# Performance work log

Hardware: AMD Instinct MI355X
Metric: run time of the kernel (lower is better)

## Reference

```python
import jax, jax.numpy as jnp
import numpy as np

T, B, K, N, M = 1024, 32, 8, 64, 64
DELTA = 3  # number of passes: DELTA-1 states-only + 1 final with output


def setup_inputs():
    key = jax.random.key(0)
    ks = jax.random.split(key, 7)
    x = jax.random.normal(ks[0], (T, B, K), jnp.float32)
    # stable, a.s.-distinct complex eigenvalues: |lam| in [0.5, 0.99)
    mag = jax.random.uniform(ks[1], (K, N), jnp.float32, 0.5, 0.99)
    phase = jax.random.uniform(ks[2], (K, N), jnp.float32, -np.pi, np.pi)
    lam_re = mag * jnp.cos(phase)
    lam_im = mag * jnp.sin(phase)
    C_re = jax.random.normal(ks[3], (K, N, M), jnp.float32) / np.sqrt(N)
    C_im = jax.random.normal(ks[4], (K, N, M), jnp.float32) / np.sqrt(N)
    D = jax.random.normal(ks[5], (K, M), jnp.float32)
    Do = jax.random.normal(ks[6], (K, M), jnp.float32)
    return {"x": x, "lam_re": lam_re, "lam_im": lam_im,
            "C_re": C_re, "C_im": C_im, "D": D, "Do": Do}


def _compute_Bp(lam):
    # Bʹ[k,j] = exp(-sum_i log(1 - lam_i/lam_j)), diagonal ratio zeroed
    k, n = lam.shape
    ratios = lam[:, :, None] / lam[:, None, :]           # (k, n, n)
    eye = jnp.eye(n, dtype=bool)[None]
    ratios = jnp.where(eye, jnp.zeros((), ratios.dtype), ratios)
    lnBp = -jnp.sum(jnp.log(1.0 - ratios), axis=1)       # (k, n)
    return jnp.exp(lnBp)


def _linear_recurrence(a, bx):
    # s_t = a_t * s_{t-1} + bx_t, computed as a parallel associative scan
    def comb(l, r):
        al, bl = l
        ar, br = r
        return (al * ar, bl * ar + br)
    _, s = jax.lax.associative_scan(comb, (a, bx), axis=0)
    return s


def _states(xc, lam, Bp, alpha):
    # one pass of the complex diagonal SSM; returns states (T, B, K, N)
    Bpx = (xc[..., None] * Bp).reshape(T, B, K * N)       # Bʹ·x
    if alpha is None:
        al = jnp.broadcast_to(lam.reshape(1, 1, K * N), (T, B, K * N))
    else:
        al = (alpha * lam[None, None]).reshape(T, B, K * N)  # α·λ
    # standard=True: shift inputs by one step (prepend zeros, drop last)
    z = jnp.zeros((1, B, K * N), al.dtype)
    al = jnp.concatenate([z, al[:-1]], axis=0)
    Bpx = jnp.concatenate([z, Bpx[:-1]], axis=0)
    return _linear_recurrence(al, Bpx).reshape(T, B, K, N)


def _forward(x, lam_re, lam_im, C_re, C_im, D, Do):
    lam = (lam_re + 1j * lam_im).astype(jnp.complex64)    # (K, N)
    Cp = (C_re + 1j * C_im).astype(jnp.complex64)         # (K, N, M)
    xc = x.astype(jnp.complex64)                          # (T, B, K)
    Bp = _compute_Bp(lam)                                 # (K, N)

    alpha = None
    for _ in range(DELTA - 1):
        s = _states(xc, lam, Bp, alpha)                   # (T, B, K, N)
        ls = lam[None, None] * s                          # λ·sʹ
        alpha = 1.0 / jnp.sqrt(1.0 + ls * jnp.conj(ls))   # recipsq

    s = _states(xc, lam, Bp, alpha)                       # final pass
    Cs = jnp.einsum("tbkn,knm->tbkm", s, Cp)              # Cʹ·sʹ
    Dx = xc[..., None] * D.astype(jnp.complex64)          # D·x
    y = Cs + Dx + Do.astype(jnp.complex64)                # (T, B, K, M)
    return jnp.mean(y, axis=2)                            # average over k


def reference(x, lam_re, lam_im, C_re, C_im, D, Do):
    return _forward(x, lam_re, lam_im, C_re, C_im, D, Do)
```

## Files before the change

### kernel.cpp

```cpp
#include <hip/hip_runtime.h>

#define TT 1024
#define BB 32
#define KKD 8
#define NN 64
#define MM 64
#define BKC (BB*KKD)
#define KN  (KKD*NN)

typedef __attribute__((ext_vector_type(8))) _Float16 f16x8;
typedef __attribute__((ext_vector_type(2))) __fp16 fp16x2;
typedef __attribute__((ext_vector_type(4))) float f32x4;

#define SC_DOWN (1.0f/4096.0f)
#define SC_UP   512.0f


static __device__ __forceinline__ float bcast(float v, int lane) {
    return __builtin_bit_cast(float,
        __builtin_amdgcn_readlane(__builtin_bit_cast(int, v), lane));
}
static __device__ __forceinline__ float f16lo(unsigned int pk) {
    return (float)__builtin_bit_cast(_Float16, (unsigned short)(pk & 0xffffu));
}
static __device__ __forceinline__ float f16hi(unsigned int pk) {
    return (float)__builtin_bit_cast(_Float16, (unsigned short)(pk >> 16));
}

__global__ __launch_bounds__(64) void bp_kernel(const float* __restrict__ lam_re,
                                                const float* __restrict__ lam_im,
                                                float* __restrict__ bp) {
    int k = blockIdx.x;
    int j = threadIdx.x;
    double ljre = (double)lam_re[k*NN+j], ljim = (double)lam_im[k*NN+j];
    double dj = ljre*ljre + ljim*ljim;
    double pre = 1.0, pim = 0.0;
    for (int i = 0; i < NN; ++i) {
        if (i == j) continue;
        double lire = (double)lam_re[k*NN+i], liim = (double)lam_im[k*NN+i];
        double rre = (lire*ljre + liim*ljim)/dj;
        double rim = (liim*ljre - lire*ljim)/dj;
        double zre = 1.0 - rre, zim = -rim;
        double zd = zre*zre + zim*zim;
        double npre = (pre*zre + pim*zim)/zd;
        double npim = (pim*zre - pre*zim)/zd;
        pre = npre; pim = npim;
    }
    bp[(k*NN+j)*2+0] = (float)pre;
    bp[(k*NN+j)*2+1] = (float)pim;
}

__global__ __launch_bounds__(256) void wprep_kernel(const float* __restrict__ C_re,
                                                    const float* __restrict__ C_im,
                                                    unsigned short* __restrict__ Wt) {
    int idx = blockIdx.x*256 + threadIdx.x;
    int m  = idx >> 10;
    int j  = idx & 1023;
    int kn = j >> 1;
    float v = (j & 1) ? -C_im[kn*MM + m] : C_re[kn*MM + m];
    Wt[idx] = __builtin_bit_cast(unsigned short, (_Float16)(v * SC_UP));
}

__global__ __launch_bounds__(512, 8) void scan_par5_kernel(const float* __restrict__ x,
                                                           const float* __restrict__ lam_re,
                                                           const float* __restrict__ lam_im,
                                                           const float* __restrict__ bp,
                                                           unsigned int* __restrict__ abuf,
                                                           int TL) {
    __shared__ float e[32][16][2];
    __shared__ float pa[32][16];
    __shared__ unsigned int apk[32][16][17];

    int blk = blockIdx.x;
    int bk = blk >> 2;
    int q2 = blk & 3;
    int b = bk >> 3;
    int k = bk & 7;
    int tid = threadIdx.x;
    int seg = tid >> 4;
    int nl  = tid & 15;
    int n   = q2*16 + nl;
    int kn  = k*NN + n;

    float lre = lam_re[kn], lim = lam_im[kn];
    float bpre = bp[2*kn+0], bpim = bp[2*kn+1];
    float l2 = lre*lre + lim*lim;

    float p32re = lre, p32im = lim;
    #pragma unroll
    for (int i = 0; i < 5; ++i) {
        float tr = p32re*p32re - p32im*p32im;
        float ti = 2.f*p32re*p32im;
        p32re = tr; p32im = ti;
    }

    float xs0 = x[(size_t)(seg*32 + nl)*BKC + b*KKD + k];
    float xs1 = x[(size_t)(seg*32 + 16 + nl)*BKC + b*KKD + k];

    float s1re = 0.f, s1im = 0.f;
    #pragma unroll
    for (int i = 0; i < 32; ++i) {
        float xv = (i < 16) ? __shfl(xs0, i, 16) : __shfl(xs1, i - 16, 16);
        float ure = xv*bpre, uim = xv*bpim;
        float tre = __builtin_fmaf(lre, s1re, __builtin_fmaf(-lim, s1im, ure));
        float tim = __builtin_fmaf(lre, s1im, __builtin_fmaf( lim, s1re, uim));
        s1re = tre; s1im = tim;
    }
    e[seg][nl][0] = s1re; e[seg][nl][1] = s1im;
    __syncthreads();
    float c1re = 0.f, c1im = 0.f;
    for (int i = 0; i < seg; ++i) {
        float tre = __builtin_fmaf(p32re, c1re, __builtin_fmaf(-p32im, c1im, e[i][nl][0]));
        float tim = __builtin_fmaf(p32re, c1im, __builtin_fmaf( p32im, c1re, e[i][nl][1]));
        c1re = tre; c1im = tim;
    }
    __syncthreads();

    s1re = c1re; s1im = c1im;
    float s2re = 0.f, s2im = 0.f, pav = 1.f;
    float a1prev = 0.f;
    #pragma unroll
    for (int i = 0; i < 32; ++i) {
        float xv = (i < 16) ? __shfl(xs0, i, 16) : __shfl(xs1, i - 16, 16);
        float ure = xv*bpre, uim = xv*bpim;
        float mm1 = __builtin_fmaf(l2, __builtin_fmaf(s1re, s1re, s1im*s1im), 1.f);
        float a1 = rsqrtf(mm1);
        float t1re = __builtin_fmaf(lre, s1re, __builtin_fmaf(-lim, s1im, ure));
        float t1im = __builtin_fmaf(lre, s1im, __builtin_fmaf( lim, s1re, uim));
        s1re = t1re; s1im = t1im;
        float cr = a1*lre, ci = a1*lim;
        float t2re = __builtin_fmaf(cr, s2re, __builtin_fmaf(-ci, s2im, ure));
        float t2im = __builtin_fmaf(cr, s2im, __builtin_fmaf( ci, s2re, uim));
        s2re = t2re; s2im = t2im;
        pav *= a1;
        if (i & 1)
            apk[seg][i>>1][nl] = __builtin_bit_cast(unsigned int,
                                   __builtin_amdgcn_cvt_pkrtz(a1prev, a1));
        else
            a1prev = a1;
    }
    e[seg][nl][0] = s2re; e[seg][nl][1] = s2im; pa[seg][nl] = pav;
    __syncthreads();
    float c2re = 0.f, c2im = 0.f;
    for (int i = 0; i < seg; ++i) {
        float pai = pa[i][nl];
        float qre = pai*p32re, qim = pai*p32im;
        float tre = __builtin_fmaf(qre, c2re, __builtin_fmaf(-qim, c2im, e[i][nl][0]));
        float tim = __builtin_fmaf(qre, c2im, __builtin_fmaf( qim, c2re, e[i][nl][1]));
        c2re = tre; c2im = tim;
    }
    __syncthreads();

    s2re = c2re; s2im = c2im;
    float s3re = 0.f, s3im = 0.f, pb = 1.f;
    float a2prev = 0.f;
    unsigned int pk = 0;
    #pragma unroll
    for (int i = 0; i < 32; ++i) {
        if (!(i & 1)) pk = apk[seg][i>>1][nl];
        float a1 = (i & 1) ? f16hi(pk) : f16lo(pk);
        float xv = (i < 16) ? __shfl(xs0, i, 16) : __shfl(xs1, i - 16, 16);
        float ure = xv*bpre, uim = xv*bpim;
        float mm2 = __builtin_fmaf(l2, __builtin_fmaf(s2re, s2re, s2im*s2im), 1.f);
        float a2 = rsqrtf(mm2);
        float cr = a1*lre, ci = a1*lim;
        float t2re = __builtin_fmaf(cr, s2re, __builtin_fmaf(-ci, s2im, ure));
        float t2im = __builtin_fmaf(cr, s2im, __builtin_fmaf( ci, s2re, uim));
        s2re = t2re; s2im = t2im;
        float dr = a2*lre, di = a2*lim;
        float t3re = __builtin_fmaf(dr, s3re, __builtin_fmaf(-di, s3im, ure));
        float t3im = __builtin_fmaf(dr, s3im, __builtin_fmaf( di, s3re, uim));
        s3re = t3re; s3im = t3im;
        pb *= a2;
        if (i & 1)
            apk[seg][i>>1][nl] = __builtin_bit_cast(unsigned int,
                                   __builtin_amdgcn_cvt_pkrtz(a2prev, a2));
        else
            a2prev = a2;
    }
    e[seg][nl][0] = s3re; e[seg][nl][1] = s3im; pa[seg][nl] = pb;
    __syncthreads();
    float c3re = 0.f, c3im = 0.f;
    for (int i = 0; i < seg; ++i) {
        float pbi = pa[i][nl];
        float qre = pbi*p32re, qim = pbi*p32im;
        float tre = __builtin_fmaf(qre, c3re, __builtin_fmaf(-qim, c3im, e[i][nl][0]));
        float tim = __builtin_fmaf(qre, c3im, __builtin_fmaf( qim, c3re, e[i][nl][1]));
        c3re = tre; c3im = tim;
    }

    s3re = c3re; s3im = c3im;
    unsigned int* ap = abuf + (size_t)(bk*4 + q2)*((size_t)TL*16)
                     + (seg >> 2)*2048 + (seg & 3)*16 + nl;
    #pragma unroll
    for (int i = 0; i < 32; ++i) {
        fp16x2 hv = __builtin_amdgcn_cvt_pkrtz(s3re*SC_DOWN, s3im*SC_DOWN);
        ap[(size_t)i * 64] = __builtin_bit_cast(unsigned int, hv);
        if (!(i & 1)) pk = apk[seg][i>>1][nl];
        float a2 = (i & 1) ? f16hi(pk) : f16lo(pk);
        float xv = (i < 16) ? __shfl(xs0, i, 16) : __shfl(xs1, i - 16, 16);
        float ure = xv*bpre, uim = xv*bpim;
        float dr = a2*lre, di = a2*lim;
        float t3re = __builtin_fmaf(dr, s3re, __builtin_fmaf(-di, s3im, ure));
        float t3im = __builtin_fmaf(dr, s3im, __builtin_fmaf( di, s3re, uim));
        s3re = t3re; s3im = t3im;
    }
}

__global__ __launch_bounds__(64) void scan_seq_kernel(const float* __restrict__ x,
                                                      const float* __restrict__ lam_re,
                                                      const float* __restrict__ lam_im,
                                                      const float* __restrict__ bp,
                                                      float* __restrict__ state,
                                                      unsigned int* __restrict__ abuf,
                                                      int chunk_start, int chunk_len,
                                                      int TL) {
    int bk = blockIdx.x;
    int b = bk >> 3;
    int k = bk & 7;
    int n = threadIdx.x;
    int kn = k*NN + n;
    float lre = lam_re[kn], lim = lam_im[kn];
    float bpre = bp[2*kn+0], bpim = bp[2*kn+1];
    float l2 = lre*lre + lim*lim;
    int chain = bk*NN + n;

    float s1re,s1im,s2re,s2im,s3re,s3im;
    if (chunk_start == 0) {
        s1re=s1im=s2re=s2im=s3re=s3im=0.f;
    } else {
        const float* st = state + (size_t)chain*6;
        s1re=st[0];s1im=st[1];s2re=st[2];s2im=st[3];s3re=st[4];s3im=st[5];
    }

    const float* xp = x + (size_t)chunk_start*BKC + b*KKD + k;
    int q2_ = n >> 4, nl_ = n & 15;
    unsigned int* ab = abuf + (size_t)(bk*4 + q2_)*((size_t)TL*16) + nl_;

    float xs = xp[(size_t)n * BKC];
    for (int t0 = 0; t0 < chunk_len; t0 += 64) {
        float xs_nxt = 0.f;
        if (t0 + 64 < chunk_len) xs_nxt = xp[(size_t)(t0 + 64 + n) * BKC];
        #pragma unroll
        for (int w = 0; w < 4; ++w) {
            float mm_[16], cre[16], cim[16];
            #pragma unroll
            for (int j = 0; j < 16; ++j) {
                float xv = bcast(xs, w*16 + j);
                mm_[j] = __builtin_fmaf(l2, s1re*s1re + s1im*s1im, 1.0f);
                float ure = xv*bpre, uim = xv*bpim;
                float tre = __builtin_fmaf(lre, s1re, __builtin_fmaf(-lim, s1im, ure));
                float tim = __builtin_fmaf(lre, s1im, __builtin_fmaf( lim, s1re, uim));
                s1re=tre; s1im=tim;
            }
            #pragma unroll
            for (int j = 0; j < 16; ++j) {
                float a = rsqrtf(mm_[j]); cre[j] = a*lre; cim[j] = a*lim;
            }
            #pragma unroll
            for (int j = 0; j < 16; ++j) {
                float xv = bcast(xs, w*16 + j);
                mm_[j] = __builtin_fmaf(l2, s2re*s2re + s2im*s2im, 1.0f);
                float ure = xv*bpre, uim = xv*bpim;
                float tre = __builtin_fmaf(cre[j], s2re, __builtin_fmaf(-cim[j], s2im, ure));
                float tim = __builtin_fmaf(cre[j], s2im, __builtin_fmaf( cim[j], s2re, uim));
                s2re=tre; s2im=tim;
            }
            #pragma unroll
            for (int j = 0; j < 16; ++j) {
                float a = rsqrtf(mm_[j]); cre[j] = a*lre; cim[j] = a*lim;
            }
            #pragma unroll
            for (int j = 0; j < 16; ++j) {
                int t = t0 + w*16 + j;
                fp16x2 hv = __builtin_amdgcn_cvt_pkrtz(s3re*SC_DOWN, s3im*SC_DOWN);
                ab[((size_t)(t >> 7))*2048 + (t & 31)*64 + ((t >> 5) & 3)*16]
                    = __builtin_bit_cast(unsigned int, hv);
                float xv = bcast(xs, w*16 + j);
                float ure = xv*bpre, uim = xv*bpim;
                float tre = __builtin_fmaf(cre[j], s3re, __builtin_fmaf(-cim[j], s3im, ure));
                float tim = __builtin_fmaf(cre[j], s3im, __builtin_fmaf( cim[j], s3re, uim));
                s3re=tre; s3im=tim;
            }
        }
        xs = xs_nxt;
    }
    float* st = state + (size_t)chain*6;
    st[0]=s1re;st[1]=s1im;st[2]=s2re;st[3]=s2im;st[4]=s3re;st[5]=s3im;
}

__global__ __launch_bounds__(256) void proj_kernel(const unsigned int* __restrict__ A,
                                                   const unsigned short* __restrict__ Wt,
                                                   const float* __restrict__ x,
                                                   const float* __restrict__ D,
                                                   const float* __restrict__ Do,
                                                   float* __restrict__ out,
                                                   int rowOff, int TL) {
    __shared__ uint4 At[2][1024];
    __shared__ uint4 Wb[2][1024];
    int tid = threadIdx.x;
    int w = tid >> 6, l = tid & 63;
    int lg = l >> 4, lr = l & 15;
    int wr = w >> 1, wc = w & 1;
    int bI = blockIdx.x;
    int t0 = ((bI >> 5) << 6) + (bI & 31);
    size_t TLQ = (size_t)TL * 16;

    f32x4 acc[2][2];
    #pragma unroll
    for (int g = 0; g < 2; ++g)
        #pragma unroll
        for (int t = 0; t < 2; ++t) acc[g][t] = (f32x4){0.f,0.f,0.f,0.f};

    uint4 ra[4], rw[4];
    int srow[4], su[4];
    #pragma unroll
    for (int i = 0; i < 4; ++i) {
        int unit = w*256 + i*64 + l;
        srow[i] = unit >> 4;
        su[i]   = unit & 15;
    }

    #pragma unroll
    for (int i = 0; i < 4; ++i) {
        int row = srow[i], u = su[i];
        int b = row & 31, t2 = t0 + ((row >> 5) << 5);
        size_t idx = (size_t)((b*8 + 0)*4 + (u >> 2))*TLQ
                   + (size_t)(t2 >> 7)*2048 + (t2 & 31)*64 + ((t2 >> 5) & 3)*16 + (u & 3)*4;
        ra[i] = *(const uint4*)(A + idx);
        rw[i] = *(const uint4*)((const char*)Wt + (row*2048 + 0*256 + u*16));
    }
    #pragma unroll
    for (int i = 0; i < 4; ++i) {
        int row = srow[i], u = su[i];
        At[0][row*16 + (u ^ (row & 7))] = ra[i];
        Wb[0][row*16 + (u ^ (row & 7))] = rw[i];
    }
    __syncthreads();

    for (int kc = 0; kc < 8; ++kc) {
        int cur = kc & 1;
        if (kc < 7) {
            int kn = kc + 1;
            #pragma unroll
            for (int i = 0; i < 4; ++i) {
                int row = srow[i], u = su[i];
                int b = row & 31, t2 = t0 + ((row >> 5) << 5);
                size_t idx = (size_t)((b*8 + kn)*4 + (u >> 2))*TLQ
                           + (size_t)(t2 >> 7)*2048 + (t2 & 31)*64 + ((t2 >> 5) & 3)*16 + (u & 3)*4;
                ra[i] = *(const uint4*)(A + idx);
                rw[i] = *(const uint4*)((const char*)Wt + (row*2048 + kn*256 + u*16));
            }
        }
        #pragma unroll
        for (int ks = 0; ks < 4; ++ks) {
            f16x8 af[2], bf[2];
            #pragma unroll
            for (int g = 0; g < 2; ++g) {
                int row = (wr*2 + g)*16 + lr;
                af[g] = __builtin_bit_cast(f16x8, At[cur][row*16 + ((ks*4 + lg) ^ (row & 7))]);
            }
            #pragma unroll
            for (int t = 0; t < 2; ++t) {
                int m = (wc*2 + t)*16 + lr;
                bf[t] = __builtin_bit_cast(f16x8, Wb[cur][m*16 + ((ks*4 + lg) ^ (m & 7))]);
            }
            #pragma unroll
            for (int g = 0; g < 2; ++g)
                #pragma unroll
                for (int t = 0; t < 2; ++t)
                    acc[g][t] = __builtin_amdgcn_mfma_f32_16x16x32_f16(af[g], bf[t], acc[g][t], 0,0,0);
        }
        if (kc < 7) {
            int nb = (kc + 1) & 1;
            #pragma unroll
            for (int i = 0; i < 4; ++i) {
                int row = srow[i], u = su[i];
                At[nb][row*16 + (u ^ (row & 7))] = ra[i];
                Wb[nb][row*16 + (u ^ (row & 7))] = rw[i];
            }
        }
        __syncthreads();
    }

    #pragma unroll
    for (int g = 0; g < 2; ++g) {
        int row_o = (wr*2 + g)*16 + lr;
        int grow = rowOff + (t0 + ((row_o >> 5) << 5))*32 + (row_o & 31);
        const float* xr = x + (size_t)grow * KKD;
        float4 x0 = *(const float4*)(xr);
        float4 x1 = *(const float4*)(xr + 4);
        f16x8 a2;
        a2[0] = (lg==0) ? (_Float16)x0.x : ((lg==1) ? (_Float16)1.0f : (_Float16)0.0f);
        a2[1] = (lg==0) ? (_Float16)x0.y : (_Float16)0.0f;
        a2[2] = (lg==0) ? (_Float16)x0.z : (_Float16)0.0f;
        a2[3] = (lg==0) ? (_Float16)x0.w : (_Float16)0.0f;
        a2[4] = (lg==0) ? (_Float16)x1.x : (_Float16)0.0f;
        a2[5] = (lg==0) ? (_Float16)x1.y : (_Float16)0.0f;
        a2[6] = (lg==0) ? (_Float16)x1.z : (_Float16)0.0f;
        a2[7] = (lg==0) ? (_Float16)x1.w : (_Float16)0.0f;
        #pragma unroll
        for (int t = 0; t < 2; ++t) {
            int c = (wc*2 + t)*16 + lr;
            float dob = 0.f;
            #pragma unroll
            for (int i = 0; i < 8; ++i) dob += Do[i*64 + c];
            f16x8 b2;
            b2[0] = (lg==0) ? (_Float16)(D[0*64+c]*0.125f)
                  : ((lg==1) ? (_Float16)(dob*0.125f) : (_Float16)0.0f);
            b2[1] = (lg==0) ? (_Float16)(D[1*64+c]*0.125f) : (_Float16)0.0f;
            b2[2] = (lg==0) ? (_Float16)(D[2*64+c]*0.125f) : (_Float16)0.0f;
            b2[3] = (lg==0) ? (_Float16)(D[3*64+c]*0.125f) : (_Float16)0.0f;
            b2[4] = (lg==0) ? (_Float16)(D[4*64+c]*0.125f) : (_Float16)0.0f;
            b2[5] = (lg==0) ? (_Float16)(D[5*64+c]*0.125f) : (_Float16)0.0f;
            b2[6] = (lg==0) ? (_Float16)(D[6*64+c]*0.125f) : (_Float16)0.0f;
            b2[7] = (lg==0) ? (_Float16)(D[7*64+c]*0.125f) : (_Float16)0.0f;
            acc[g][t] = __builtin_amdgcn_mfma_f32_16x16x32_f16(a2, b2, acc[g][t], 0,0,0);
        }
    }

    #pragma unroll
    for (int g = 0; g < 2; ++g)
        #pragma unroll
        for (int t = 0; t < 2; ++t) {
            int c = (wc*2 + t)*16 + lr;
            #pragma unroll
            for (int reg = 0; reg < 4; ++reg) {
                int row_o = (wr*2 + g)*16 + lg*4 + reg;
                int grow = rowOff + (t0 + ((row_o >> 5) << 5))*32 + (row_o & 31);
                out[(size_t)grow*MM + c] = acc[g][t][reg];
            }
        }
}

extern "C" void kernel_launch(void* const* d_in, const int* in_sizes, int n_in,
                              void* d_out, int out_size, void* d_ws, size_t ws_size,
                              hipStream_t stream) {
    const float* x      = (const float*)d_in[0];
    const float* lam_re = (const float*)d_in[1];
    const float* lam_im = (const float*)d_in[2];
    const float* C_re   = (const float*)d_in[3];
    const float* C_im   = (const float*)d_in[4];
    const float* D      = (const float*)d_in[5];
    const float* Do     = (const float*)d_in[6];
    float* out = (float*)d_out;

    char* ws = (char*)d_ws;
    float*          bpw    = (float*)(ws);
    unsigned short* Wt     = (unsigned short*)(ws + 4096);
    float*          statew = (float*)(ws + 135168);
    unsigned int*   abuf   = (unsigned int*)(ws + 528384);

    bp_kernel<<<KKD, NN, 0, stream>>>(lam_re, lam_im, bpw);
    wprep_kernel<<<256, 256, 0, stream>>>(C_re, C_im, Wt);

    const size_t base = 528384;
    const size_t perT = (size_t)BB*KN*4;

    if (ws_size >= base + (size_t)TT*perT) {
        scan_par5_kernel<<<BKC*4, 512, 0, stream>>>(x, lam_re, lam_im, bpw, abuf, TT);
        proj_kernel<<<TT*BB/64, 256, 0, stream>>>(abuf, Wt, x, D, Do, out, 0, TT);
    } else {
        size_t avail = ws_size > base ? ws_size - base : 0;
        int chunkT = (int)(avail / perT) & ~127;
        if (chunkT < 128) chunkT = 128;
        for (int cs = 0; cs < TT; cs += chunkT) {
            int len = (chunkT < TT - cs) ? chunkT : (TT - cs);
            scan_seq_kernel<<<BKC, NN, 0, stream>>>(x, lam_re, lam_im, bpw, statew,
                                                    abuf, cs, len, len);
            proj_kernel<<<len*BB/64, 256, 0, stream>>>(abuf, Wt, x, D, Do, out,
                                                       cs*BB, len);
        }
    }
}
```

Baseline: 74.70 us.

## Load projection weights directly from global in MFMA layout and deepen A prefetch

The weight prep kernel now writes C in an MFMA-fragment-friendly order, so the projection kernel reads B fragments straight from global/L2 instead of staging them in shared memory. The A tile uses a triple shared buffer with a two-stage register prefetch, issuing loads two chunks ahead to hide latency. This cuts shared memory use and LDS writes, but adds per-iteration global loads for weights inside the MFMA loop and more registers.

```diff
diff --git a/kernel.cpp b/kernel.cpp
--- a/kernel.cpp
+++ b/kernel.cpp
@@ -55,10 +55,12 @@
                                                     unsigned short* __restrict__ Wt) {
     int idx = blockIdx.x*256 + threadIdx.x;
     int m  = idx >> 10;
-    int j  = idx & 1023;
-    int kn = j >> 1;
-    float v = (j & 1) ? -C_im[kn*MM + m] : C_re[kn*MM + m];
-    Wt[idx] = __builtin_bit_cast(unsigned short, (_Float16)(v * SC_UP));
+    int c  = idx & 1023;
+    int kn = c >> 1;
+    float v = (c & 1) ? -C_im[kn*MM + m] : C_re[kn*MM + m];
+    int kc = c >> 7, ks = (c >> 5) & 3, lg = (c >> 3) & 3, e = c & 7;
+    int idx2 = (((kc*4 + ks)*4 + lg)*64 + m)*8 + e;
+    Wt[idx2] = __builtin_bit_cast(unsigned short, (_Float16)(v * SC_UP));
 }
 
 __global__ __launch_bounds__(512, 8) void scan_par5_kernel(const float* __restrict__ x,
@@ -296,8 +298,7 @@
                                                    const float* __restrict__ Do,
                                                    float* __restrict__ out,
                                                    int rowOff, int TL) {
-    __shared__ uint4 At[2][1024];
-    __shared__ uint4 Wb[2][1024];
+    __shared__ uint4 At[3][1024];
     int tid = threadIdx.x;
     int w = tid >> 6, l = tid & 63;
     int lg = l >> 4, lr = l & 15;
@@ -312,7 +313,7 @@
         #pragma unroll
         for (int t = 0; t < 2; ++t) acc[g][t] = (f32x4){0.f,0.f,0.f,0.f};
 
-    uint4 ra[4], rw[4];
+    uint4 ra[2][4];
     int srow[4], su[4];
     #pragma unroll
     for (int i = 0; i < 4; ++i) {
@@ -321,49 +322,42 @@
         su[i]   = unit & 15;
     }
 
+    size_t abase[4];
     #pragma unroll
     for (int i = 0; i < 4; ++i) {
         int row = srow[i], u = su[i];
         int b = row & 31, t2 = t0 + ((row >> 5) << 5);
-        size_t idx = (size_t)((b*8 + 0)*4 + (u >> 2))*TLQ
-                   + (size_t)(t2 >> 7)*2048 + (t2 & 31)*64 + ((t2 >> 5) & 3)*16 + (u & 3)*4;
-        ra[i] = *(const uint4*)(A + idx);
-        rw[i] = *(const uint4*)((const char*)Wt + (row*2048 + 0*256 + u*16));
-    }
+        abase[i] = (size_t)(b*8*4 + (u >> 2))*TLQ
+                 + (size_t)(t2 >> 7)*2048 + (t2 & 31)*64 + ((t2 >> 5) & 3)*16 + (u & 3)*4;
+    }
+    size_t kstep = (size_t)4 * TLQ;
+
+    #pragma unroll
+    for (int i = 0; i < 4; ++i) ra[0][i] = *(const uint4*)(A + abase[i]);
+    #pragma unroll
+    for (int i = 0; i < 4; ++i) ra[1][i] = *(const uint4*)(A + abase[i] + kstep);
     #pragma unroll
     for (int i = 0; i < 4; ++i) {
         int row = srow[i], u = su[i];
-        At[0][row*16 + (u ^ (row & 7))] = ra[i];
-        Wb[0][row*16 + (u ^ (row & 7))] = rw[i];
+        At[0][row*16 + (u ^ (row & 7))] = ra[0][i];
     }
     __syncthreads();
 
     for (int kc = 0; kc < 8; ++kc) {
-        int cur = kc & 1;
-        if (kc < 7) {
-            int kn = kc + 1;
-            #pragma unroll
-            for (int i = 0; i < 4; ++i) {
-                int row = srow[i], u = su[i];
-                int b = row & 31, t2 = t0 + ((row >> 5) << 5);
-                size_t idx = (size_t)((b*8 + kn)*4 + (u >> 2))*TLQ
-                           + (size_t)(t2 >> 7)*2048 + (t2 & 31)*64 + ((t2 >> 5) & 3)*16 + (u & 3)*4;
-                ra[i] = *(const uint4*)(A + idx);
-                rw[i] = *(const uint4*)((const char*)Wt + (row*2048 + kn*256 + u*16));
-            }
-        }
+        int cb = kc % 3;
         #pragma unroll
         for (int ks = 0; ks < 4; ++ks) {
             f16x8 af[2], bf[2];
             #pragma unroll
             for (int g = 0; g < 2; ++g) {
                 int row = (wr*2 + g)*16 + lr;
-                af[g] = __builtin_bit_cast(f16x8, At[cur][row*16 + ((ks*4 + lg) ^ (row & 7))]);
+                af[g] = __builtin_bit_cast(f16x8, At[cb][row*16 + ((ks*4 + lg) ^ (row & 7))]);
             }
             #pragma unroll
             for (int t = 0; t < 2; ++t) {
                 int m = (wc*2 + t)*16 + lr;
-                bf[t] = __builtin_bit_cast(f16x8, Wb[cur][m*16 + ((ks*4 + lg) ^ (m & 7))]);
+                const unsigned short* bp_ = Wt + (size_t)(((kc*4 + ks)*4 + lg)*64 + m)*8;
+                bf[t] = __builtin_bit_cast(f16x8, *(const uint4*)bp_);
             }
             #pragma unroll
             for (int g = 0; g < 2; ++g)
@@ -372,13 +366,17 @@
                     acc[g][t] = __builtin_amdgcn_mfma_f32_16x16x32_f16(af[g], bf[t], acc[g][t], 0,0,0);
         }
         if (kc < 7) {
-            int nb = (kc + 1) & 1;
+            int nb = (kc + 1) % 3;
             #pragma unroll
             for (int i = 0; i < 4; ++i) {
                 int row = srow[i], u = su[i];
-                At[nb][row*16 + (u ^ (row & 7))] = ra[i];
-                Wb[nb][row*16 + (u ^ (row & 7))] = rw[i];
-            }
+                At[nb][row*16 + (u ^ (row & 7))] = ra[(kc + 1) & 1][i];
+            }
+        }
+        if (kc < 6) {
+            #pragma unroll
+            for (int i = 0; i < 4; ++i)
+                ra[kc & 1][i] = *(const uint4*)(A + abase[i] + (size_t)(kc + 2)*kstep);
         }
         __syncthreads();
     }
```

New measurement: 89.05 us. 1.19x slower.
